# Kernel optimization log

Hardware: AMD Instinct MI355X
Metric: run time of the kernel (lower is better)

## Reference

```python
import jax, jax.numpy as jnp
import numpy as np
import math

B, L, D, H = 2, 2048, 1024, 16

def setup_inputs() -> dict:
    key = jax.random.key(0)
    ks = jax.random.split(key, 5)
    return {
        "query": jax.random.normal(ks[0], (B, L, D), dtype=jnp.float32),
        "key": jax.random.normal(ks[1], (B, L, D), dtype=jnp.float32),
        "value": jax.random.normal(ks[2], (B, L, D), dtype=jnp.float32),
        "w_out": jax.random.normal(ks[3], (D, D), dtype=jnp.float32) * (1.0 / math.sqrt(D)),
        "b_out": jnp.zeros((D,), dtype=jnp.float32),
    }

def reference(query, key, value, w_out, b_out):
    b, l, d_model = query.shape
    num_heads = H
    head_dim = d_model // num_heads
    scaling = 1.0 / math.sqrt(d_model)  # NOTE: module scales by embed_dim, not head_dim

    def reshape(x):
        return x.reshape(b, l, num_heads, head_dim).transpose(0, 2, 1, 3)  # [B,H,L,hd]

    q, k, v = reshape(query), reshape(key), reshape(value)
    scores = jnp.einsum("bhqd,bhkd->bhqk", q, k) * scaling  # [B,H,L,L]

    u = max(1, int(math.ceil(math.log(l + 1))))  # static: 8 for L=2048
    _, topk_idx = jax.lax.top_k(scores, u)  # [B,H,L,u]

    # scatter True at top-u key positions per query
    bi = jnp.arange(b)[:, None, None, None]
    hi = jnp.arange(num_heads)[None, :, None, None]
    qi = jnp.arange(l)[None, None, :, None]
    mask = jnp.zeros(scores.shape, dtype=bool).at[bi, hi, qi, topk_idx].set(True)

    scores_masked = jnp.where(mask, scores, -jnp.inf)
    attn_weights = jax.nn.softmax(scores_masked, axis=-1)  # [B,H,L,L]

    attn_out = jnp.einsum("bhqk,bhkd->bhqd", attn_weights, v)
    attn_out = attn_out.transpose(0, 2, 1, 3).reshape(b, l, d_model)
    attn_out = attn_out @ w_out.T + b_out  # nn.Linear
    return attn_out, attn_weights
```

## Files before the change

kernel.cpp:

```cpp
#include <hip/hip_runtime.h>
#include <math.h>

#define BB 2
#define LL 2048
#define DD 1024
#define HH 16
#define SCALE 0.03125f

#define ATTN_ELEMS ((size_t)BB * LL * DD)

typedef unsigned short u16;
typedef __attribute__((ext_vector_type(8))) short bf16x8;
typedef __attribute__((ext_vector_type(4))) short s16x4;
typedef __attribute__((ext_vector_type(4))) float f32x4;

__device__ __forceinline__ u16 f2bf_rne(float f) {
    union { float f; unsigned u; } c; c.f = f;
    unsigned u = c.u;
    u += 0x7fffu + ((u >> 16) & 1u);
    return (u16)(u >> 16);
}

__device__ __forceinline__ void splitbf(float x, short& h, short& l) {
    union { float f; unsigned u; } c; c.f = x;
    unsigned uh = c.u & 0xFFFF0000u;
    h = (short)(uh >> 16);
    union { unsigned u; float f; } ch; ch.u = uh;
    l = (short)f2bf_rne(x - ch.f);
}

__device__ __forceinline__ void insert8(float (&tv)[8], int (&ti)[8], float cv, int ci) {
    bool g0 = cv > tv[0], g1 = cv > tv[1], g2 = cv > tv[2], g3 = cv > tv[3],
         g4 = cv > tv[4], g5 = cv > tv[5], g6 = cv > tv[6];
    tv[7] = g6 ? tv[6] : cv;                 ti[7] = g6 ? ti[6] : ci;
    tv[6] = g5 ? tv[5] : (g6 ? cv : tv[6]);  ti[6] = g5 ? ti[5] : (g6 ? ci : ti[6]);
    tv[5] = g4 ? tv[4] : (g5 ? cv : tv[5]);  ti[5] = g4 ? ti[4] : (g5 ? ci : ti[5]);
    tv[4] = g3 ? tv[3] : (g4 ? cv : tv[4]);  ti[4] = g3 ? ti[3] : (g4 ? ci : ti[4]);
    tv[3] = g2 ? tv[2] : (g3 ? cv : tv[3]);  ti[3] = g2 ? ti[2] : (g3 ? ci : ti[3]);
    tv[2] = g1 ? tv[1] : (g2 ? cv : tv[2]);  ti[2] = g1 ? ti[1] : (g2 ? ci : ti[2]);
    tv[1] = g0 ? tv[0] : (g1 ? cv : tv[1]);  ti[1] = g0 ? ti[0] : (g1 ? ci : ti[1]);
    tv[0] = g0 ? cv : tv[0];                 ti[0] = g0 ? ci : ti[0];
}

__device__ __forceinline__ void insert8t(float (&tv)[8], int (&ti)[8], float cv, int ci) {
    bool g0 = cv > tv[0] || (cv == tv[0] && ci < ti[0]);
    bool g1 = cv > tv[1] || (cv == tv[1] && ci < ti[1]);
    bool g2 = cv > tv[2] || (cv == tv[2] && ci < ti[2]);
    bool g3 = cv > tv[3] || (cv == tv[3] && ci < ti[3]);
    bool g4 = cv > tv[4] || (cv == tv[4] && ci < ti[4]);
    bool g5 = cv > tv[5] || (cv == tv[5] && ci < ti[5]);
    bool g6 = cv > tv[6] || (cv == tv[6] && ci < ti[6]);
    tv[7] = g6 ? tv[6] : cv;                 ti[7] = g6 ? ti[6] : ci;
    tv[6] = g5 ? tv[5] : (g6 ? cv : tv[6]);  ti[6] = g5 ? ti[5] : (g6 ? ci : ti[6]);
    tv[5] = g4 ? tv[4] : (g5 ? cv : tv[5]);  ti[5] = g4 ? ti[4] : (g5 ? ci : ti[5]);
    tv[4] = g3 ? tv[3] : (g4 ? cv : tv[4]);  ti[4] = g3 ? ti[3] : (g4 ? ci : ti[4]);
    tv[3] = g2 ? tv[2] : (g3 ? cv : tv[3]);  ti[3] = g2 ? ti[2] : (g3 ? ci : ti[3]);
    tv[2] = g1 ? tv[1] : (g2 ? cv : tv[2]);  ti[2] = g1 ? ti[1] : (g2 ? ci : ti[2]);
    tv[1] = g0 ? tv[0] : (g1 ? cv : tv[1]);  ti[1] = g0 ? ti[0] : (g1 ? ci : ti[1]);
    tv[0] = g0 ? cv : tv[0];                 ti[0] = g0 ? ci : ti[0];
}

__device__ __forceinline__ void insert12(float (&tv)[12], int (&ti)[12], float cv, int ci) {
    bool g0 = cv > tv[0], g1 = cv > tv[1], g2 = cv > tv[2], g3 = cv > tv[3],
         g4 = cv > tv[4], g5 = cv > tv[5], g6 = cv > tv[6], g7 = cv > tv[7],
         g8 = cv > tv[8], g9 = cv > tv[9], g10 = cv > tv[10];
    tv[11] = g10 ? tv[10] : cv;                 ti[11] = g10 ? ti[10] : ci;
    tv[10] = g9 ? tv[9] : (g10 ? cv : tv[10]);  ti[10] = g9 ? ti[9] : (g10 ? ci : ti[10]);
    tv[9]  = g8 ? tv[8] : (g9 ? cv : tv[9]);    ti[9]  = g8 ? ti[8] : (g9 ? ci : ti[9]);
    tv[8]  = g7 ? tv[7] : (g8 ? cv : tv[8]);    ti[8]  = g7 ? ti[7] : (g8 ? ci : ti[8]);
    tv[7]  = g6 ? tv[6] : (g7 ? cv : tv[7]);    ti[7]  = g6 ? ti[6] : (g7 ? ci : ti[7]);
    tv[6]  = g5 ? tv[5] : (g6 ? cv : tv[6]);    ti[6]  = g5 ? ti[5] : (g6 ? ci : ti[6]);
    tv[5]  = g4 ? tv[4] : (g5 ? cv : tv[5]);    ti[5]  = g4 ? ti[4] : (g5 ? ci : ti[5]);
    tv[4]  = g3 ? tv[3] : (g4 ? cv : tv[4]);    ti[4]  = g3 ? ti[3] : (g4 ? ci : ti[4]);
    tv[3]  = g2 ? tv[2] : (g3 ? cv : tv[3]);    ti[3]  = g2 ? ti[2] : (g3 ? ci : ti[3]);
    tv[2]  = g1 ? tv[1] : (g2 ? cv : tv[2]);    ti[2]  = g1 ? ti[1] : (g2 ? ci : ti[2]);
    tv[1]  = g0 ? tv[0] : (g1 ? cv : tv[1]);    ti[1]  = g0 ? ti[0] : (g1 ? ci : ti[1]);
    tv[0]  = g0 ? cv : tv[0];                   ti[0]  = g0 ? ci : ti[0];
}

__device__ __forceinline__ void merge4(
    const float* v0, const int* i0, const float* v1, const int* i1,
    const float* v2, const int* i2, const float* v3, const int* i3,
    float* ov, int* oi)
{
    int p0 = 0, p1 = 0, p2 = 0, p3 = 0;
    #pragma unroll
    for (int s = 0; s < 8; ++s) {
        float a0 = v0[p0], a1 = v1[p1], a2 = v2[p2], a3 = v3[p3];
        int   b0 = i0[p0], b1 = i1[p1], b2 = i2[p2], b3 = i3[p3];
        float bv = a0; int bi = b0; int bc = 0;
        if (a1 > bv || (a1 == bv && b1 < bi)) { bv = a1; bi = b1; bc = 1; }
        if (a2 > bv || (a2 == bv && b2 < bi)) { bv = a2; bi = b2; bc = 2; }
        if (a3 > bv || (a3 == bv && b3 < bi)) { bv = a3; bi = b3; bc = 3; }
        p0 += (bc == 0); p1 += (bc == 1); p2 += (bc == 2); p3 += (bc == 3);
        ov[s] = bv; oi[s] = bi;
    }
}


__global__ __launch_bounds__(256) void prep_k_kernel(
    const float* __restrict__ k, u16* __restrict__ khi, u16* __restrict__ klo)
{
    int gid = blockIdx.x * 256 + threadIdx.x;
    int li   = gid & 15;
    int qd   = (gid >> 4) & 3;
    int c    = (gid >> 6) & 1;
    int s    = (gid >> 7) & 127;
    int head = gid >> 14;
    int b = head >> 4, h = head & 15;
    const float* src = k + ((size_t)(b * LL + s * 16 + li)) * DD + h * 64 + c * 32 + qd * 8;
    float x[8];
    *(f32x4*)x       = *(const f32x4*)src;
    *(f32x4*)(x + 4) = *(const f32x4*)(src + 4);
    bf16x8 h8, l8;
    #pragma unroll
    for (int e = 0; e < 8; ++e) { short hh, ll; splitbf(x[e], hh, ll); h8[e] = hh; l8[e] = ll; }
    *(bf16x8*)&khi[(size_t)gid * 8] = h8;
    *(bf16x8*)&klo[(size_t)gid * 8] = l8;
}

__global__ __launch_bounds__(256) void prep_w_kernel(
    const float* __restrict__ w, u16* __restrict__ whi, u16* __restrict__ wlo)
{
    int gid = blockIdx.x * 256 + threadIdx.x;
    int li = gid & 15;
    int qd = (gid >> 4) & 3;
    int c  = (gid >> 6) & 3;
    int nt = (gid >> 8) & 3;
    int kc = (gid >> 10) & 7;
    int nb = gid >> 13;
    const float* src = w + (size_t)(nb * 64 + nt * 16 + li) * DD + kc * 128 + c * 32 + qd * 8;
    float x[8];
    *(f32x4*)x       = *(const f32x4*)src;
    *(f32x4*)(x + 4) = *(const f32x4*)(src + 4);
    bf16x8 h8, l8;
    #pragma unroll
    for (int e = 0; e < 8; ++e) { short hh, ll; splitbf(x[e], hh, ll); h8[e] = hh; l8[e] = ll; }
    *(bf16x8*)&whi[(size_t)gid * 8] = h8;
    *(bf16x8*)&wlo[(size_t)gid * 8] = l8;
}

__global__ __launch_bounds__(256, 4) void attn_fast_kernel(
    const float* __restrict__ q, const float* __restrict__ k, const float* __restrict__ v,
    const u16* __restrict__ khi_g, const u16* __restrict__ klo_g,
    float* __restrict__ aw, u16* __restrict__ chi, u16* __restrict__ clo)
{
    const int swz  = (blockIdx.x & 7) * 128 + (blockIdx.x >> 3);
    const int qt   = swz & 31;
    const int h    = (swz >> 5) & 15;
    const int b    = swz >> 9;
    const int t    = threadIdx.x;
    const int wv   = t >> 6;
    const int lane = t & 63;
    const int li   = lane & 15;
    const int quad = lane >> 4;

    __shared__ __align__(16) char arena[21504];
    u16*   gsel = (u16*)(arena);
    float* dv   = (float*)(arena + 1536);
    u16*   dg   = (u16*)(arena + 13824);
    float* s2v  = (float*)(arena + 1536);
    u16*   s2i  = (u16*)(arena + 13824);
    float* wrow = (float*)(arena + 18432);
    u16*   wixs = (u16*)(arena + 20480);

    f32x4* awz = (f32x4*)(aw + (((size_t)(b * HH + h) * LL) + (size_t)qt * 64) * LL);
    const f32x4 zero4 = {0.f, 0.f, 0.f, 0.f};

    bf16x8 qh0, ql0, qh1, ql1;
    {
        const float* qrow = q + ((size_t)(b * LL + qt * 64 + wv * 16 + li)) * DD + h * 64;
        float x[8];
        *(f32x4*)x       = *(const f32x4*)(qrow + quad * 8);
        *(f32x4*)(x + 4) = *(const f32x4*)(qrow + quad * 8 + 4);
        #pragma unroll
        for (int e = 0; e < 8; ++e) { short hh, ll; splitbf(x[e], hh, ll); qh0[e] = hh; ql0[e] = ll; }
        *(f32x4*)x       = *(const f32x4*)(qrow + 32 + quad * 8);
        *(f32x4*)(x + 4) = *(const f32x4*)(qrow + 32 + quad * 8 + 4);
        #pragma unroll
        for (int e = 0; e < 8; ++e) { short hh, ll; splitbf(x[e], hh, ll); qh1[e] = hh; ql1[e] = ll; }
    }

    float tv[12]; int tg[12];
    #pragma unroll
    for (int s = 0; s < 12; ++s) { tv[s] = -INFINITY; tg[s] = 0; }

    const u16* khb = khi_g + (size_t)(b * HH + h) * 131072 + (size_t)lane * 8;
    const u16* klb = klo_g + (size_t)(b * HH + h) * 131072 + (size_t)lane * 8;

    bf16x8 Ah0 = *(const bf16x8*)(khb);
    bf16x8 Ah1 = *(const bf16x8*)(khb + 512);
    bf16x8 Al0 = *(const bf16x8*)(klb);
    bf16x8 Al1 = *(const bf16x8*)(klb + 512);
    bf16x8 Bh0 = *(const bf16x8*)(khb + 1024);
    bf16x8 Bh1 = *(const bf16x8*)(khb + 1536);
    bf16x8 Bl0 = *(const bf16x8*)(klb + 1024);
    bf16x8 Bl1 = *(const bf16x8*)(klb + 1536);

    #pragma unroll 2
    for (int sp = 0; sp < 64; ++sp) {
        const int spn = (sp + 1) & 63;
        const size_t off = (size_t)spn * 2048;
        bf16x8 NAh0 = *(const bf16x8*)(khb + off);
        bf16x8 NAh1 = *(const bf16x8*)(khb + off + 512);
        bf16x8 NAl0 = *(const bf16x8*)(klb + off);
        bf16x8 NAl1 = *(const bf16x8*)(klb + off + 512);
        bf16x8 NBh0 = *(const bf16x8*)(khb + off + 1024);
        bf16x8 NBh1 = *(const bf16x8*)(khb + off + 1536);
        bf16x8 NBl0 = *(const bf16x8*)(klb + off + 1024);
        bf16x8 NBl1 = *(const bf16x8*)(klb + off + 1536);

        awz[sp * 512 + t]       = zero4;
        awz[sp * 512 + 256 + t] = zero4;

        f32x4 c4a = {0,0,0,0}, c4b = {0,0,0,0}, d4a = {0,0,0,0}, d4b = {0,0,0,0};
        c4a = __builtin_amdgcn_mfma_f32_16x16x32_bf16(Ah0, qh0, c4a, 0, 0, 0);
        c4b = __builtin_amdgcn_mfma_f32_16x16x32_bf16(Ah1, qh1, c4b, 0, 0, 0);
        d4a = __builtin_amdgcn_mfma_f32_16x16x32_bf16(Bh0, qh0, d4a, 0, 0, 0);
        d4b = __builtin_amdgcn_mfma_f32_16x16x32_bf16(Bh1, qh1, d4b, 0, 0, 0);
        c4a = __builtin_amdgcn_mfma_f32_16x16x32_bf16(Al0, qh0, c4a, 0, 0, 0);
        c4b = __builtin_amdgcn_mfma_f32_16x16x32_bf16(Al1, qh1, c4b, 0, 0, 0);
        d4a = __builtin_amdgcn_mfma_f32_16x16x32_bf16(Bl0, qh0, d4a, 0, 0, 0);
        d4b = __builtin_amdgcn_mfma_f32_16x16x32_bf16(Bl1, qh1, d4b, 0, 0, 0);
        c4a = __builtin_amdgcn_mfma_f32_16x16x32_bf16(Ah0, ql0, c4a, 0, 0, 0);
        c4b = __builtin_amdgcn_mfma_f32_16x16x32_bf16(Ah1, ql1, c4b, 0, 0, 0);
        d4a = __builtin_amdgcn_mfma_f32_16x16x32_bf16(Bh0, ql0, d4a, 0, 0, 0);
        d4b = __builtin_amdgcn_mfma_f32_16x16x32_bf16(Bh1, ql1, d4b, 0, 0, 0);

        float s0 = c4a[0] + c4b[0], s1 = c4a[1] + c4b[1];
        float s2 = c4a[2] + c4b[2], s3 = c4a[3] + c4b[3];
        float s4 = d4a[0] + d4b[0], s5 = d4a[1] + d4b[1];
        float s6 = d4a[2] + d4b[2], s7 = d4a[3] + d4b[3];
        float m = fmaxf(fmaxf(fmaxf(s0, s1), fmaxf(s2, s3)),
                        fmaxf(fmaxf(s4, s5), fmaxf(s6, s7)));
        if (m > tv[11]) insert12(tv, tg, m, sp * 32 + quad * 4);

        Ah0 = NAh0; Ah1 = NAh1; Al0 = NAl0; Al1 = NAl1;
        Bh0 = NBh0; Bh1 = NBh1; Bl0 = NBl0; Bl1 = NBl1;
    }

    {
        const int row = wv * 16 + li;
        #pragma unroll
        for (int s = 0; s < 12; ++s) {
            dv[row * 48 + quad * 12 + s] = tv[s];
            dg[row * 48 + quad * 12 + s] = (u16)tg[s];
        }
    }
    __syncthreads();

    if (t < 64) {
        const float* v0 = &dv[t * 48];       const u16* i0 = &dg[t * 48];
        const float* v1 = &dv[t * 48 + 12];  const u16* i1 = &dg[t * 48 + 12];
        const float* v2 = &dv[t * 48 + 24];  const u16* i2 = &dg[t * 48 + 24];
        const float* v3 = &dv[t * 48 + 36];  const u16* i3 = &dg[t * 48 + 36];
        int p0 = 0, p1 = 0, p2 = 0, p3 = 0;
        #pragma unroll
        for (int s = 0; s < 12; ++s) {
            float a0 = v0[p0], a1 = v1[p1], a2 = v2[p2], a3 = v3[p3];
            int   b0 = i0[p0], b1 = i1[p1], b2 = i2[p2], b3 = i3[p3];
            float bv = a0; int bi = b0; int bc = 0;
            if (a1 > bv || (a1 == bv && b1 < bi)) { bv = a1; bi = b1; bc = 1; }
            if (a2 > bv || (a2 == bv && b2 < bi)) { bv = a2; bi = b2; bc = 2; }
            if (a3 > bv || (a3 == bv && b3 < bi)) { bv = a3; bi = b3; bc = 3; }
            p0 += (bc == 0); p1 += (bc == 1); p2 += (bc == 2); p3 += (bc == 3);
            gsel[t * 12 + s] = (u16)bi;
        }
    }
    __syncthreads();

    {
        const int row = t >> 2, p = t & 3;
        const float* qp = q + ((size_t)(b * LL + qt * 64 + row)) * DD + h * 64;
        f32x4 qr[16];
        #pragma unroll
        for (int d4 = 0; d4 < 16; ++d4) qr[d4] = *(const f32x4*)(qp + d4 * 4);
        float tv8[8]; int ti8[8];
        #pragma unroll
        for (int s = 0; s < 8; ++s) { tv8[s] = -INFINITY; ti8[s] = 0x7fffffff; }
        for (int jj = 0; jj < 24; jj += 2) {
            int gk = (int)gsel[row * 12 + p * 3 + (jj >> 3)];
            int e  = jj & 7;
            int k0 = gk + ((e >> 2) << 4) + (e & 3);
            int k1 = k0 + 1;
            const float* kp0 = k + ((size_t)(b * LL + k0)) * DD + h * 64;
            const float* kp1 = k + ((size_t)(b * LL + k1)) * DD + h * 64;
            float a0 = 0.f, a1 = 0.f, a2 = 0.f, a3 = 0.f;
            float b0 = 0.f, b1 = 0.f, b2 = 0.f, b3 = 0.f;
            #pragma unroll
            for (int d4 = 0; d4 < 16; ++d4) {
                f32x4 ka = *(const f32x4*)(kp0 + d4 * 4);
                f32x4 kb = *(const f32x4*)(kp1 + d4 * 4);
                a0 = fmaf(qr[d4][0], ka[0], a0);
                a1 = fmaf(qr[d4][1], ka[1], a1);
                a2 = fmaf(qr[d4][2], ka[2], a2);
                a3 = fmaf(qr[d4][3], ka[3], a3);
                b0 = fmaf(qr[d4][0], kb[0], b0);
                b1 = fmaf(qr[d4][1], kb[1], b1);
                b2 = fmaf(qr[d4][2], kb[2], b2);
                b3 = fmaf(qr[d4][3], kb[3], b3);
            }
            float sc0 = ((a0 + a1) + (a2 + a3)) * SCALE;
            float sc1 = ((b0 + b1) + (b2 + b3)) * SCALE;
            if (sc0 > tv8[7] || (sc0 == tv8[7] && k0 < ti8[7])) insert8t(tv8, ti8, sc0, k0);
            if (sc1 > tv8[7] || (sc1 == tv8[7] && k1 < ti8[7])) insert8t(tv8, ti8, sc1, k1);
        }
        #pragma unroll
        for (int s = 0; s < 8; ++s) {
            s2v[(row * 4 + p) * 9 + s] = tv8[s];
            s2i[(row * 4 + p) * 9 + s] = (u16)ti8[s];
        }
    }
    __syncthreads();

    if (t < 64) {
        const float* v0 = &s2v[(t * 4 + 0) * 9]; const u16* i0 = &s2i[(t * 4 + 0) * 9];
        const float* v1 = &s2v[(t * 4 + 1) * 9]; const u16* i1 = &s2i[(t * 4 + 1) * 9];
        const float* v2 = &s2v[(t * 4 + 2) * 9]; const u16* i2 = &s2i[(t * 4 + 2) * 9];
        const float* v3 = &s2v[(t * 4 + 3) * 9]; const u16* i3 = &s2i[(t * 4 + 3) * 9];
        int p0 = 0, p1 = 0, p2 = 0, p3 = 0;
        float fv[8]; int fi[8];
        #pragma unroll
        for (int s = 0; s < 8; ++s) {
            float a0 = v0[p0], a1 = v1[p1], a2 = v2[p2], a3 = v3[p3];
            int   b0 = i0[p0], b1 = i1[p1], b2 = i2[p2], b3 = i3[p3];
            float bv = a0; int bi = b0; int bc = 0;
            if (a1 > bv || (a1 == bv && b1 < bi)) { bv = a1; bi = b1; bc = 1; }
            if (a2 > bv || (a2 == bv && b2 < bi)) { bv = a2; bi = b2; bc = 2; }
            if (a3 > bv || (a3 == bv && b3 < bi)) { bv = a3; bi = b3; bc = 3; }
            p0 += (bc == 0); p1 += (bc == 1); p2 += (bc == 2); p3 += (bc == 3);
            fv[s] = bv; fi[s] = bi;
        }
        float m = fv[0];
        float e0[8]; float sum = 0.f;
        #pragma unroll
        for (int s = 0; s < 8; ++s) { e0[s] = __expf(fv[s] - m); sum += e0[s]; }
        float inv = 1.0f / sum;
        float* awrow = aw + (((size_t)(b * HH + h) * LL) + (size_t)qt * 64 + t) * LL;
        #pragma unroll
        for (int s = 0; s < 8; ++s) {
            float w8 = e0[s] * inv;
            awrow[fi[s]] = w8;
            wrow[t * 8 + s] = w8; wixs[t * 8 + s] = (u16)fi[s];
        }
    }
    __syncthreads();

    const float* vbase = v + ((size_t)b * LL) * DD + h * 64;
    #pragma unroll
    for (int i = 0; i < 4; ++i) {
        int id = i * 256 + t;
        int row = id >> 4, seg = id & 15;
        f32x4 acc = {0.f, 0.f, 0.f, 0.f};
        #pragma unroll
        for (int s = 0; s < 8; ++s) {
            float ws = wrow[row * 8 + s];
            f32x4 vvv = *(const f32x4*)(vbase + (size_t)wixs[row * 8 + s] * DD + seg * 4);
            acc[0] = fmaf(ws, vvv[0], acc[0]);
            acc[1] = fmaf(ws, vvv[1], acc[1]);
            acc[2] = fmaf(ws, vvv[2], acc[2]);
            acc[3] = fmaf(ws, vvv[3], acc[3]);
        }
        size_t off = ((size_t)(b * LL + qt * 64 + row)) * DD + h * 64 + seg * 4;
        s16x4 h4, l4;
        #pragma unroll
        for (int j = 0; j < 4; ++j) { short hh, ll; splitbf(acc[j], hh, ll); h4[j] = hh; l4[j] = ll; }
        *(s16x4*)(chi + off) = h4;
        *(s16x4*)(clo + off) = l4;
    }
}

__global__ __launch_bounds__(256) void linear_fast_kernel(
    const u16* __restrict__ chi, const u16* __restrict__ clo,
    const u16* __restrict__ whi, const u16* __restrict__ wlo,
    const float* __restrict__ bias, float* __restrict__ out)
{
    const int bid  = blockIdx.x;
    const int nb   = bid & 15, mb = bid >> 4;
    const int t    = threadIdx.x;
    const int wv   = t >> 6;
    const int lane = t & 63;
    const int li   = lane & 15;
    const int quad = lane >> 4;

    f32x4 acc0 = {0.f,0.f,0.f,0.f}, acc1 = {0.f,0.f,0.f,0.f},
          acc2 = {0.f,0.f,0.f,0.f}, acc3 = {0.f,0.f,0.f,0.f};

    const u16* ah_row = chi + (size_t)(mb * 64 + wv * 16 + li) * DD + quad * 8;
    const u16* al_row = clo + (size_t)(mb * 64 + wv * 16 + li) * DD + quad * 8;
    const size_t wboff = (size_t)nb * 65536 + (size_t)lane * 8;

    for (int kc = 0; kc < 8; ++kc) {
        const u16* wb_h = whi + wboff + kc * 8192;
        const u16* wb_l = wlo + wboff + kc * 8192;
        #pragma unroll
        for (int c = 0; c < 4; ++c) {
            bf16x8 ah = *(const bf16x8*)(ah_row + kc * 128 + c * 32);
            bf16x8 al = *(const bf16x8*)(al_row + kc * 128 + c * 32);
            bf16x8 bh0 = *(const bf16x8*)(wb_h + c * 512);
            bf16x8 bl0 = *(const bf16x8*)(wb_l + c * 512);
            bf16x8 bh1 = *(const bf16x8*)(wb_h + 2048 + c * 512);
            bf16x8 bl1 = *(const bf16x8*)(wb_l + 2048 + c * 512);
            bf16x8 bh2 = *(const bf16x8*)(wb_h + 4096 + c * 512);
            bf16x8 bl2 = *(const bf16x8*)(wb_l + 4096 + c * 512);
            bf16x8 bh3 = *(const bf16x8*)(wb_h + 6144 + c * 512);
            bf16x8 bl3 = *(const bf16x8*)(wb_l + 6144 + c * 512);
            acc0 = __builtin_amdgcn_mfma_f32_16x16x32_bf16(ah, bh0, acc0, 0, 0, 0);
            acc0 = __builtin_amdgcn_mfma_f32_16x16x32_bf16(ah, bl0, acc0, 0, 0, 0);
            acc0 = __builtin_amdgcn_mfma_f32_16x16x32_bf16(al, bh0, acc0, 0, 0, 0);
            acc1 = __builtin_amdgcn_mfma_f32_16x16x32_bf16(ah, bh1, acc1, 0, 0, 0);
            acc1 = __builtin_amdgcn_mfma_f32_16x16x32_bf16(ah, bl1, acc1, 0, 0, 0);
            acc1 = __builtin_amdgcn_mfma_f32_16x16x32_bf16(al, bh1, acc1, 0, 0, 0);
            acc2 = __builtin_amdgcn_mfma_f32_16x16x32_bf16(ah, bh2, acc2, 0, 0, 0);
            acc2 = __builtin_amdgcn_mfma_f32_16x16x32_bf16(ah, bl2, acc2, 0, 0, 0);
            acc2 = __builtin_amdgcn_mfma_f32_16x16x32_bf16(al, bh2, acc2, 0, 0, 0);
            acc3 = __builtin_amdgcn_mfma_f32_16x16x32_bf16(ah, bh3, acc3, 0, 0, 0);
            acc3 = __builtin_amdgcn_mfma_f32_16x16x32_bf16(ah, bl3, acc3, 0, 0, 0);
            acc3 = __builtin_amdgcn_mfma_f32_16x16x32_bf16(al, bh3, acc3, 0, 0, 0);
        }
    }

    #pragma unroll
    for (int st = 0; st < 4; ++st) {
        f32x4 a = (st == 0) ? acc0 : (st == 1) ? acc1 : (st == 2) ? acc2 : acc3;
        int col = nb * 64 + st * 16 + li;
        float bb2 = bias[col];
        #pragma unroll
        for (int r = 0; r < 4; ++r)
            out[(size_t)(mb * 64 + wv * 16 + quad * 4 + r) * DD + col] = a[r] + bb2;
    }
}


__global__ __launch_bounds__(256) void attn_kernel(
    const float* __restrict__ q, const float* __restrict__ k, const float* __restrict__ v,
    float* __restrict__ aw, float* __restrict__ ctx)
{
    const int bid  = blockIdx.x;
    const int qt   = bid & 31;
    const int h    = (bid >> 5) & 15;
    const int b    = bid >> 9;
    const int t    = threadIdx.x;
    const int wv   = t >> 6;
    const int lane = t & 63;
    const int li   = lane & 15;
    const int quad = lane >> 4;

    __shared__ __align__(16) char smA[32768];
    __shared__ float s2v[32][4][8];
    __shared__ int   s2i[32][4][8];
    __shared__ int   cidx[32][12];
    __shared__ float cs[32][12];
    __shared__ float wrow[64][8];
    __shared__ int   wix[64][8];
    u16* khi = (u16*)smA;
    u16* klo = (u16*)(smA + 16384);

    const float* kbase = k + ((size_t)b * LL) * DD + h * 64;
    f32x4* awz = (f32x4*)(aw + (((size_t)(b * HH + h) * LL) + (size_t)qt * 64) * LL);
    const f32x4 zero4 = {0.f, 0.f, 0.f, 0.f};

    bf16x8 qh0, ql0, qh1, ql1;
    {
        const float* qrow = q + ((size_t)(b * LL + qt * 64 + wv * 16 + li)) * DD + h * 64;
        float x[8];
        *(f32x4*)x       = *(const f32x4*)(qrow + quad * 8);
        *(f32x4*)(x + 4) = *(const f32x4*)(qrow + quad * 8 + 4);
        #pragma unroll
        for (int e = 0; e < 8; ++e) { short hh, ll; splitbf(x[e], hh, ll); qh0[e] = hh; ql0[e] = ll; }
        *(f32x4*)x       = *(const f32x4*)(qrow + 32 + quad * 8);
        *(f32x4*)(x + 4) = *(const f32x4*)(qrow + 32 + quad * 8 + 4);
        #pragma unroll
        for (int e = 0; e < 8; ++e) { short hh, ll; splitbf(x[e], hh, ll); qh1[e] = hh; ql1[e] = ll; }
    }

    float tv[4][8]; int tix[4][8];
    #pragma unroll
    for (int r = 0; r < 4; ++r)
        #pragma unroll
        for (int s = 0; s < 8; ++s) { tv[r][s] = -INFINITY; tix[r][s] = 0; }

    for (int iter = 0; iter < 16; ++iter) {
        __syncthreads();
        #pragma unroll
        for (int j = 0; j < 4; ++j) {
            int f   = j * 256 + t;
            int col = f >> 3;
            int c   = (f >> 2) & 1;
            int qd  = f & 3;
            const float* src = kbase + (size_t)(iter * 128 + col) * DD + c * 32 + qd * 8;
            float x[8];
            *(f32x4*)x       = *(const f32x4*)src;
            *(f32x4*)(x + 4) = *(const f32x4*)(src + 4);
            bf16x8 h8, l8;
            #pragma unroll
            for (int e = 0; e < 8; ++e) { short hh, ll; splitbf(x[e], hh, ll); h8[e] = hh; l8[e] = ll; }
            int off = (((col >> 4) * 2 + c) << 9) + (qd << 7) + ((col & 15) << 3);
            *(bf16x8*)&khi[off] = h8;
            *(bf16x8*)&klo[off] = l8;
        }
        #pragma unroll
        for (int i = 0; i < 8; ++i) awz[iter * 2048 + i * 256 + t] = zero4;
        __syncthreads();

        #pragma unroll
        for (int s = 0; s < 8; ++s) {
            int fo = s << 10;
            bf16x8 kh0 = *(bf16x8*)&khi[fo + (lane << 3)];
            bf16x8 kh1 = *(bf16x8*)&khi[fo + 512 + (lane << 3)];
            bf16x8 kl0 = *(bf16x8*)&klo[fo + (lane << 3)];
            bf16x8 kl1 = *(bf16x8*)&klo[fo + 512 + (lane << 3)];
            f32x4 c4 = {0.f, 0.f, 0.f, 0.f};
            c4 = __builtin_amdgcn_mfma_f32_16x16x32_bf16(qh0, kh0, c4, 0, 0, 0);
            c4 = __builtin_amdgcn_mfma_f32_16x16x32_bf16(qh1, kh1, c4, 0, 0, 0);
            c4 = __builtin_amdgcn_mfma_f32_16x16x32_bf16(qh0, kl0, c4, 0, 0, 0);
            c4 = __builtin_amdgcn_mfma_f32_16x16x32_bf16(qh1, kl1, c4, 0, 0, 0);
            c4 = __builtin_amdgcn_mfma_f32_16x16x32_bf16(ql0, kh0, c4, 0, 0, 0);
            c4 = __builtin_amdgcn_mfma_f32_16x16x32_bf16(ql1, kh1, c4, 0, 0, 0);
            int ci = iter * 128 + s * 16 + li;
            #pragma unroll
            for (int r = 0; r < 4; ++r) {
                float cv = c4[r] * SCALE;
                if (cv > tv[r][7]) insert8(tv[r], tix[r], cv, ci);
            }
        }
    }

    float* mv = (float*)smA;
    int*   mi = (int*)(smA + 16384);
    for (int bb = 0; bb < 2; ++bb) {
        __syncthreads();
        if ((wv >> 1) == bb) {
            int rl0 = (wv & 1) * 16 + quad * 4;
            #pragma unroll
            for (int r = 0; r < 4; ++r) {
                int base = (rl0 + r) * 128 + li * 8;
                #pragma unroll
                for (int s = 0; s < 8; ++s) { mv[base + s] = tv[r][s]; mi[base + s] = tix[r][s]; }
            }
        }
        __syncthreads();
        if (t < 128) {
            int rr = t >> 2, p = t & 3;
            int base = rr * 128 + p * 32;
            merge4(&mv[base], &mi[base], &mv[base + 8], &mi[base + 8],
                   &mv[base + 16], &mi[base + 16], &mv[base + 24], &mi[base + 24],
                   s2v[rr][p], s2i[rr][p]);
        }
        __syncthreads();
        if (t < 32) {
            int rr = t;
            int pp[4] = {0, 0, 0, 0};
            #pragma unroll
            for (int s = 0; s < 12; ++s) {
                float bv = -INFINITY; int bi = 0x7fffffff; int bc = 0;
                #pragma unroll
                for (int l = 0; l < 4; ++l) {
                    if (pp[l] < 8) {
                        float hv = s2v[rr][l][pp[l]]; int hi2 = s2i[rr][l][pp[l]];
                        if (hv > bv || (hv == bv && hi2 < bi)) { bv = hv; bi = hi2; bc = l; }
                    }
                }
                pp[bc] += 1;
                cidx[rr][s] = bi;
            }
        }
        __syncthreads();
        for (int task = t; task < 384; task += 256) {
            int row = task / 12, c = task - row * 12;
            const float* qp = q + ((size_t)(b * LL + qt * 64 + bb * 32 + row)) * DD + h * 64;
            const float* kp = k + ((size_t)(b * LL + cidx[row][c])) * DD + h * 64;
            float acc = 0.f;
            for (int d4 = 0; d4 < 16; ++d4) {
                f32x4 qa = *(const f32x4*)(qp + d4 * 4);
                f32x4 ka = *(const f32x4*)(kp + d4 * 4);
                acc = fmaf(qa[0], ka[0], acc);
                acc = fmaf(qa[1], ka[1], acc);
                acc = fmaf(qa[2], ka[2], acc);
                acc = fmaf(qa[3], ka[3], acc);
            }
            cs[row][c] = acc * SCALE;
        }
        __syncthreads();
        if (t < 32) {
            int rr = t;
            float vv[12]; int ii[12];
            #pragma unroll
            for (int c = 0; c < 12; ++c) { vv[c] = cs[rr][c]; ii[c] = cidx[rr][c]; }
            float fv[8]; int fi[8];
            #pragma unroll
            for (int s = 0; s < 8; ++s) {
                float bv = -INFINITY; int bi = 0x7fffffff; int bc = 0;
                #pragma unroll
                for (int c = 0; c < 12; ++c) {
                    if (vv[c] > bv || (vv[c] == bv && ii[c] < bi)) { bv = vv[c]; bi = ii[c]; bc = c; }
                }
                vv[bc] = -INFINITY;
                fv[s] = bv; fi[s] = bi;
            }
            float m = fv[0];
            float e0[8]; float sum = 0.f;
            #pragma unroll
            for (int s = 0; s < 8; ++s) { e0[s] = __expf(fv[s] - m); sum += e0[s]; }
            float inv = 1.0f / sum;
            int grow = bb * 32 + rr;
            float* awrow = aw + (((size_t)(b * HH + h) * LL) + (size_t)qt * 64 + grow) * LL;
            #pragma unroll
            for (int s = 0; s < 8; ++s) {
                float w8 = e0[s] * inv;
                awrow[fi[s]] = w8;
                wrow[grow][s] = w8; wix[grow][s] = fi[s];
            }
        }
    }
    __syncthreads();

    const float* vbase = v + ((size_t)b * LL) * DD + h * 64;
    #pragma unroll
    for (int i = 0; i < 4; ++i) {
        int id = i * 256 + t;
        int row = id >> 4, seg = id & 15;
        f32x4 acc = {0.f, 0.f, 0.f, 0.f};
        #pragma unroll
        for (int s = 0; s < 8; ++s) {
            float ws = wrow[row][s];
            f32x4 vvv = *(const f32x4*)(vbase + (size_t)wix[row][s] * DD + seg * 4);
            acc[0] = fmaf(ws, vvv[0], acc[0]);
            acc[1] = fmaf(ws, vvv[1], acc[1]);
            acc[2] = fmaf(ws, vvv[2], acc[2]);
            acc[3] = fmaf(ws, vvv[3], acc[3]);
        }
        *(f32x4*)(ctx + ((size_t)(b * LL + qt * 64 + row)) * DD + h * 64 + seg * 4) = acc;
    }
}

__global__ __launch_bounds__(256) void linear_ws_kernel(
    const float* __restrict__ ctx, const float* __restrict__ w,
    const float* __restrict__ bias, float* __restrict__ out)
{
    const int bid  = blockIdx.x;
    const int nb   = bid & 15, mb = bid >> 4;
    const int t    = threadIdx.x;
    const int wv   = t >> 6;
    const int lane = t & 63;
    const int li   = lane & 15;
    const int quad = lane >> 4;

    __shared__ u16 bhi[8192], blo[8192];

    f32x4 acc0 = {0.f,0.f,0.f,0.f}, acc1 = {0.f,0.f,0.f,0.f},
          acc2 = {0.f,0.f,0.f,0.f}, acc3 = {0.f,0.f,0.f,0.f};
    const float* arow = ctx + (size_t)(mb * 64 + wv * 16 + li) * DD;

    for (int kc = 0; kc < 8; ++kc) {
        __syncthreads();
        #pragma unroll
        for (int j = 0; j < 4; ++j) {
            int f   = j * 256 + t;
            int col = f >> 4;
            int c   = (f >> 2) & 3;
            int qd  = f & 3;
            const float* src = w + (size_t)(nb * 64 + col) * DD + kc * 128 + c * 32 + qd * 8;
            float x[8];
            *(f32x4*)x       = *(const f32x4*)src;
            *(f32x4*)(x + 4) = *(const f32x4*)(src + 4);
            bf16x8 h8, l8;
            #pragma unroll
            for (int e = 0; e < 8; ++e) { short hh, ll; splitbf(x[e], hh, ll); h8[e] = hh; l8[e] = ll; }
            int off = (((col >> 4) * 4 + c) << 9) + (qd << 7) + ((col & 15) << 3);
            *(bf16x8*)&bhi[off] = h8;
            *(bf16x8*)&blo[off] = l8;
        }
        __syncthreads();

        bf16x8 ah[4], al[4];
        #pragma unroll
        for (int c = 0; c < 4; ++c) {
            float x[8];
            *(f32x4*)x       = *(const f32x4*)(arow + kc * 128 + c * 32 + quad * 8);
            *(f32x4*)(x + 4) = *(const f32x4*)(arow + kc * 128 + c * 32 + quad * 8 + 4);
            #pragma unroll
            for (int e = 0; e < 8; ++e) { short hh, ll; splitbf(x[e], hh, ll); ah[c][e] = hh; al[c][e] = ll; }
        }
        #pragma unroll
        for (int c = 0; c < 4; ++c) {
            bf16x8 bh0 = *(bf16x8*)&bhi[(( 0 + c) << 9) + (lane << 3)];
            bf16x8 bl0 = *(bf16x8*)&blo[(( 0 + c) << 9) + (lane << 3)];
            bf16x8 bh1 = *(bf16x8*)&bhi[(( 4 + c) << 9) + (lane << 3)];
            bf16x8 bl1 = *(bf16x8*)&blo[(( 4 + c) << 9) + (lane << 3)];
            bf16x8 bh2 = *(bf16x8*)&bhi[(( 8 + c) << 9) + (lane << 3)];
            bf16x8 bl2 = *(bf16x8*)&blo[(( 8 + c) << 9) + (lane << 3)];
            bf16x8 bh3 = *(bf16x8*)&bhi[((12 + c) << 9) + (lane << 3)];
            bf16x8 bl3 = *(bf16x8*)&blo[((12 + c) << 9) + (lane << 3)];
            acc0 = __builtin_amdgcn_mfma_f32_16x16x32_bf16(ah[c], bh0, acc0, 0, 0, 0);
            acc0 = __builtin_amdgcn_mfma_f32_16x16x32_bf16(ah[c], bl0, acc0, 0, 0, 0);
            acc0 = __builtin_amdgcn_mfma_f32_16x16x32_bf16(al[c], bh0, acc0, 0, 0, 0);
            acc1 = __builtin_amdgcn_mfma_f32_16x16x32_bf16(ah[c], bh1, acc1, 0, 0, 0);
            acc1 = __builtin_amdgcn_mfma_f32_16x16x32_bf16(ah[c], bl1, acc1, 0, 0, 0);
            acc1 = __builtin_amdgcn_mfma_f32_16x16x32_bf16(al[c], bh1, acc1, 0, 0, 0);
            acc2 = __builtin_amdgcn_mfma_f32_16x16x32_bf16(ah[c], bh2, acc2, 0, 0, 0);
            acc2 = __builtin_amdgcn_mfma_f32_16x16x32_bf16(ah[c], bl2, acc2, 0, 0, 0);
            acc2 = __builtin_amdgcn_mfma_f32_16x16x32_bf16(al[c], bh2, acc2, 0, 0, 0);
            acc3 = __builtin_amdgcn_mfma_f32_16x16x32_bf16(ah[c], bh3, acc3, 0, 0, 0);
            acc3 = __builtin_amdgcn_mfma_f32_16x16x32_bf16(ah[c], bl3, acc3, 0, 0, 0);
            acc3 = __builtin_amdgcn_mfma_f32_16x16x32_bf16(al[c], bh3, acc3, 0, 0, 0);
        }
    }

    #pragma unroll
    for (int st = 0; st < 4; ++st) {
        f32x4 a = (st == 0) ? acc0 : (st == 1) ? acc1 : (st == 2) ? acc2 : acc3;
        int col = nb * 64 + st * 16 + li;
        float bb2 = bias[col];
        #pragma unroll
        for (int r = 0; r < 4; ++r)
            out[(size_t)(mb * 64 + wv * 16 + quad * 4 + r) * DD + col] = a[r] + bb2;
    }
}

__global__ __launch_bounds__(256) void linear_inplace_kernel(
    float* io, const float* __restrict__ w, const float* __restrict__ bias)
{
    __shared__ u16 ahi[16384], alo[16384];
    const int t    = threadIdx.x;
    const int m0   = blockIdx.x * 16;
    const int wv   = t >> 6;
    const int lane = t & 63;
    const int li   = lane & 15;
    const int quad = lane >> 4;

    #pragma unroll
    for (int i = 0; i < 8; ++i) {
        int id  = i * 256 + t;
        int row = id >> 7;
        int c   = (id >> 2) & 31;
        int qd  = id & 3;
        const float* src = io + (size_t)(m0 + row) * DD + c * 32 + qd * 8;
        float x[8];
        *(f32x4*)x       = *(const f32x4*)src;
        *(f32x4*)(x + 4) = *(const f32x4*)(src + 4);
        bf16x8 h8, l8;
        #pragma unroll
        for (int e = 0; e < 8; ++e) { short hh, ll; splitbf(x[e], hh, ll); h8[e] = hh; l8[e] = ll; }
        int off = (c << 9) + (qd << 7) + (row << 3);
        *(bf16x8*)&ahi[off] = h8;
        *(bf16x8*)&alo[off] = l8;
    }
    __syncthreads();

    f32x4 acc[16];
    #pragma unroll
    for (int i = 0; i < 16; ++i) acc[i] = (f32x4){0.f, 0.f, 0.f, 0.f};

    for (int c = 0; c < 32; ++c) {
        bf16x8 ah = *(bf16x8*)&ahi[(c << 9) + (lane << 3)];
        bf16x8 al = *(bf16x8*)&alo[(c << 9) + (lane << 3)];
        #pragma unroll
        for (int sub = 0; sub < 16; ++sub) {
            int col = wv * 256 + sub * 16 + li;
            const float* src = w + (size_t)col * DD + c * 32 + quad * 8;
            float x[8];
            *(f32x4*)x       = *(const f32x4*)src;
            *(f32x4*)(x + 4) = *(const f32x4*)(src + 4);
            bf16x8 bh, bl;
            #pragma unroll
            for (int e = 0; e < 8; ++e) { short hh, ll; splitbf(x[e], hh, ll); bh[e] = hh; bl[e] = ll; }
            acc[sub] = __builtin_amdgcn_mfma_f32_16x16x32_bf16(ah, bh, acc[sub], 0, 0, 0);
            acc[sub] = __builtin_amdgcn_mfma_f32_16x16x32_bf16(ah, bl, acc[sub], 0, 0, 0);
            acc[sub] = __builtin_amdgcn_mfma_f32_16x16x32_bf16(al, bh, acc[sub], 0, 0, 0);
        }
    }

    #pragma unroll
    for (int sub = 0; sub < 16; ++sub) {
        int col = wv * 256 + sub * 16 + li;
        float bb2 = bias[col];
        #pragma unroll
        for (int r = 0; r < 4; ++r)
            io[(size_t)(m0 + quad * 4 + r) * DD + col] = acc[sub][r] + bb2;
    }
}

extern "C" void kernel_launch(void* const* d_in, const int* in_sizes, int n_in,
                              void* d_out, int out_size, void* d_ws, size_t ws_size,
                              hipStream_t stream) {
    const float* q    = (const float*)d_in[0];
    const float* k    = (const float*)d_in[1];
    const float* v    = (const float*)d_in[2];
    const float* w    = (const float*)d_in[3];
    const float* bias = (const float*)d_in[4];

    float* out = (float*)d_out;
    float* aw  = out + ATTN_ELEMS;

    const size_t CHI_ELE = ATTN_ELEMS;
    const size_t KSP_ELE = 4194304;
    const size_t WSP_ELE = 1048576;
    const size_t need_fast = (2 * CHI_ELE + 2 * KSP_ELE + 2 * WSP_ELE) * sizeof(u16);

    if (d_ws != nullptr && ws_size >= need_fast) {
        u16* chi = (u16*)d_ws;
        u16* clo = chi + CHI_ELE;
        u16* khi = clo + CHI_ELE;
        u16* klo = khi + KSP_ELE;
        u16* whi = klo + KSP_ELE;
        u16* wlo = whi + WSP_ELE;
        prep_k_kernel<<<2048, 256, 0, stream>>>(k, khi, klo);
        prep_w_kernel<<<512, 256, 0, stream>>>(w, whi, wlo);
        attn_fast_kernel<<<BB * HH * (LL / 64), 256, 0, stream>>>(q, k, v, khi, klo, aw, chi, clo);
        linear_fast_kernel<<<(BB * LL / 64) * (DD / 64), 256, 0, stream>>>(chi, clo, whi, wlo, bias, out);
    } else {
        const bool use_ws = (d_ws != nullptr) && (ws_size >= ATTN_ELEMS * sizeof(float));
        float* ctx = use_ws ? (float*)d_ws : out;
        attn_kernel<<<BB * HH * (LL / 64), 256, 0, stream>>>(q, k, v, aw, ctx);
        if (use_ws) {
            linear_ws_kernel<<<(BB * LL / 64) * (DD / 64), 256, 0, stream>>>(ctx, w, bias, out);
        } else {
            linear_inplace_kernel<<<BB * LL / 16, 256, 0, stream>>>(out, w, bias);
        }
    }
}
```

Measured before the change: 1.093 ms.

## Stage key tiles through double-buffered LDS shared by all waves

Each of the four waves previously streamed the full packed key hi/lo data from global memory on its own. Now each wave loads a quarter of every 64-key tile into a double-buffered shared-memory area, and all waves read the tile from LDS, with the next tile prefetched into registers. This cuts global/L2 traffic for keys by roughly four times, at the cost of a block barrier per tile and 32KB of shared memory. The launch-bounds occupancy hint of 4 blocks per CU is also dropped.

```diff
diff --git a/kernel.cpp b/kernel.cpp
--- a/kernel.cpp
+++ b/kernel.cpp
@@ -140,7 +140,7 @@
     *(bf16x8*)&wlo[(size_t)gid * 8] = l8;
 }
 
-__global__ __launch_bounds__(256, 4) void attn_fast_kernel(
+__global__ __launch_bounds__(256) void attn_fast_kernel(
     const float* __restrict__ q, const float* __restrict__ k, const float* __restrict__ v,
     const u16* __restrict__ khi_g, const u16* __restrict__ klo_g,
     float* __restrict__ aw, u16* __restrict__ chi, u16* __restrict__ clo)
@@ -155,14 +155,16 @@
     const int li   = lane & 15;
     const int quad = lane >> 4;
 
-    __shared__ __align__(16) char arena[21504];
-    u16*   gsel = (u16*)(arena);
-    float* dv   = (float*)(arena + 1536);
-    u16*   dg   = (u16*)(arena + 13824);
-    float* s2v  = (float*)(arena + 1536);
-    u16*   s2i  = (u16*)(arena + 13824);
-    float* wrow = (float*)(arena + 18432);
-    u16*   wixs = (u16*)(arena + 20480);
+    __shared__ __align__(16) char smem[32768];
+    u16*   kb0  = (u16*)(smem);
+    u16*   kb1  = (u16*)(smem + 16384);
+    u16*   gsel = (u16*)(smem);
+    float* dv   = (float*)(smem + 1536);
+    u16*   dg   = (u16*)(smem + 13824);
+    float* s2v  = (float*)(smem + 1536);
+    u16*   s2i  = (u16*)(smem + 13824);
+    float* wrow = (float*)(smem + 18432);
+    u16*   wixs = (u16*)(smem + 20480);
 
     f32x4* awz = (f32x4*)(aw + (((size_t)(b * HH + h) * LL) + (size_t)qt * 64) * LL);
     const f32x4 zero4 = {0.f, 0.f, 0.f, 0.f};
@@ -188,55 +190,81 @@
     const u16* khb = khi_g + (size_t)(b * HH + h) * 131072 + (size_t)lane * 8;
     const u16* klb = klo_g + (size_t)(b * HH + h) * 131072 + (size_t)lane * 8;
 
-    bf16x8 Ah0 = *(const bf16x8*)(khb);
-    bf16x8 Ah1 = *(const bf16x8*)(khb + 512);
-    bf16x8 Al0 = *(const bf16x8*)(klb);
-    bf16x8 Al1 = *(const bf16x8*)(klb + 512);
-    bf16x8 Bh0 = *(const bf16x8*)(khb + 1024);
-    bf16x8 Bh1 = *(const bf16x8*)(khb + 1536);
-    bf16x8 Bl0 = *(const bf16x8*)(klb + 1024);
-    bf16x8 Bl1 = *(const bf16x8*)(klb + 1536);
-
-    #pragma unroll 2
-    for (int sp = 0; sp < 64; ++sp) {
-        const int spn = (sp + 1) & 63;
-        const size_t off = (size_t)spn * 2048;
-        bf16x8 NAh0 = *(const bf16x8*)(khb + off);
-        bf16x8 NAh1 = *(const bf16x8*)(khb + off + 512);
-        bf16x8 NAl0 = *(const bf16x8*)(klb + off);
-        bf16x8 NAl1 = *(const bf16x8*)(klb + off + 512);
-        bf16x8 NBh0 = *(const bf16x8*)(khb + off + 1024);
-        bf16x8 NBh1 = *(const bf16x8*)(khb + off + 1536);
-        bf16x8 NBl0 = *(const bf16x8*)(klb + off + 1024);
-        bf16x8 NBl1 = *(const bf16x8*)(klb + off + 1536);
-
-        awz[sp * 512 + t]       = zero4;
-        awz[sp * 512 + 256 + t] = zero4;
-
-        f32x4 c4a = {0,0,0,0}, c4b = {0,0,0,0}, d4a = {0,0,0,0}, d4b = {0,0,0,0};
-        c4a = __builtin_amdgcn_mfma_f32_16x16x32_bf16(Ah0, qh0, c4a, 0, 0, 0);
-        c4b = __builtin_amdgcn_mfma_f32_16x16x32_bf16(Ah1, qh1, c4b, 0, 0, 0);
-        d4a = __builtin_amdgcn_mfma_f32_16x16x32_bf16(Bh0, qh0, d4a, 0, 0, 0);
-        d4b = __builtin_amdgcn_mfma_f32_16x16x32_bf16(Bh1, qh1, d4b, 0, 0, 0);
-        c4a = __builtin_amdgcn_mfma_f32_16x16x32_bf16(Al0, qh0, c4a, 0, 0, 0);
-        c4b = __builtin_amdgcn_mfma_f32_16x16x32_bf16(Al1, qh1, c4b, 0, 0, 0);
-        d4a = __builtin_amdgcn_mfma_f32_16x16x32_bf16(Bl0, qh0, d4a, 0, 0, 0);
-        d4b = __builtin_amdgcn_mfma_f32_16x16x32_bf16(Bl1, qh1, d4b, 0, 0, 0);
-        c4a = __builtin_amdgcn_mfma_f32_16x16x32_bf16(Ah0, ql0, c4a, 0, 0, 0);
-        c4b = __builtin_amdgcn_mfma_f32_16x16x32_bf16(Ah1, ql1, c4b, 0, 0, 0);
-        d4a = __builtin_amdgcn_mfma_f32_16x16x32_bf16(Bh0, ql0, d4a, 0, 0, 0);
-        d4b = __builtin_amdgcn_mfma_f32_16x16x32_bf16(Bh1, ql1, d4b, 0, 0, 0);
-
-        float s0 = c4a[0] + c4b[0], s1 = c4a[1] + c4b[1];
-        float s2 = c4a[2] + c4b[2], s3 = c4a[3] + c4b[3];
-        float s4 = d4a[0] + d4b[0], s5 = d4a[1] + d4b[1];
-        float s6 = d4a[2] + d4b[2], s7 = d4a[3] + d4b[3];
-        float m = fmaxf(fmaxf(fmaxf(s0, s1), fmaxf(s2, s3)),
-                        fmaxf(fmaxf(s4, s5), fmaxf(s6, s7)));
-        if (m > tv[11]) insert12(tv, tg, m, sp * 32 + quad * 4);
-
-        Ah0 = NAh0; Ah1 = NAh1; Al0 = NAl0; Al1 = NAl1;
-        Bh0 = NBh0; Bh1 = NBh1; Bl0 = NBl0; Bl1 = NBl1;
+    {
+        const size_t g = (size_t)wv * 1024;
+        bf16x8 r0 = *(const bf16x8*)(khb + g);
+        bf16x8 r1 = *(const bf16x8*)(khb + g + 512);
+        bf16x8 r2 = *(const bf16x8*)(klb + g);
+        bf16x8 r3 = *(const bf16x8*)(klb + g + 512);
+        u16* dst = kb0 + wv * 2048 + lane * 8;
+        *(bf16x8*)(dst)        = r0;
+        *(bf16x8*)(dst + 512)  = r1;
+        *(bf16x8*)(dst + 1024) = r2;
+        *(bf16x8*)(dst + 1536) = r3;
+    }
+    __syncthreads();
+
+    int cur = 0;
+    for (int tile = 0; tile < 32; ++tile) {
+        bf16x8 r0, r1, r2, r3;
+        const bool pf = (tile < 31);
+        if (pf) {
+            const size_t g = ((size_t)(tile + 1) * 4 + wv) * 1024;
+            r0 = *(const bf16x8*)(khb + g);
+            r1 = *(const bf16x8*)(khb + g + 512);
+            r2 = *(const bf16x8*)(klb + g);
+            r3 = *(const bf16x8*)(klb + g + 512);
+        }
+        #pragma unroll
+        for (int z = 0; z < 4; ++z) awz[tile * 1024 + z * 256 + t] = zero4;
+
+        const u16* base = cur ? kb1 : kb0;
+        #pragma unroll
+        for (int p = 0; p < 2; ++p) {
+            const int soA = (2 * p) * 2048 + lane * 8;
+            const int soB = (2 * p + 1) * 2048 + lane * 8;
+            bf16x8 Ah0 = *(const bf16x8*)(base + soA);
+            bf16x8 Ah1 = *(const bf16x8*)(base + soA + 512);
+            bf16x8 Al0 = *(const bf16x8*)(base + soA + 1024);
+            bf16x8 Al1 = *(const bf16x8*)(base + soA + 1536);
+            bf16x8 Bh0 = *(const bf16x8*)(base + soB);
+            bf16x8 Bh1 = *(const bf16x8*)(base + soB + 512);
+            bf16x8 Bl0 = *(const bf16x8*)(base + soB + 1024);
+            bf16x8 Bl1 = *(const bf16x8*)(base + soB + 1536);
+
+            f32x4 c4a = {0,0,0,0}, c4b = {0,0,0,0}, d4a = {0,0,0,0}, d4b = {0,0,0,0};
+            c4a = __builtin_amdgcn_mfma_f32_16x16x32_bf16(Ah0, qh0, c4a, 0, 0, 0);
+            c4b = __builtin_amdgcn_mfma_f32_16x16x32_bf16(Ah1, qh1, c4b, 0, 0, 0);
+            d4a = __builtin_amdgcn_mfma_f32_16x16x32_bf16(Bh0, qh0, d4a, 0, 0, 0);
+            d4b = __builtin_amdgcn_mfma_f32_16x16x32_bf16(Bh1, qh1, d4b, 0, 0, 0);
+            c4a = __builtin_amdgcn_mfma_f32_16x16x32_bf16(Al0, qh0, c4a, 0, 0, 0);
+            c4b = __builtin_amdgcn_mfma_f32_16x16x32_bf16(Al1, qh1, c4b, 0, 0, 0);
+            d4a = __builtin_amdgcn_mfma_f32_16x16x32_bf16(Bl0, qh0, d4a, 0, 0, 0);
+            d4b = __builtin_amdgcn_mfma_f32_16x16x32_bf16(Bl1, qh1, d4b, 0, 0, 0);
+            c4a = __builtin_amdgcn_mfma_f32_16x16x32_bf16(Ah0, ql0, c4a, 0, 0, 0);
+            c4b = __builtin_amdgcn_mfma_f32_16x16x32_bf16(Ah1, ql1, c4b, 0, 0, 0);
+            d4a = __builtin_amdgcn_mfma_f32_16x16x32_bf16(Bh0, ql0, d4a, 0, 0, 0);
+            d4b = __builtin_amdgcn_mfma_f32_16x16x32_bf16(Bh1, ql1, d4b, 0, 0, 0);
+
+            float s0 = c4a[0] + c4b[0], s1 = c4a[1] + c4b[1];
+            float s2 = c4a[2] + c4b[2], s3 = c4a[3] + c4b[3];
+            float s4 = d4a[0] + d4b[0], s5 = d4a[1] + d4b[1];
+            float s6 = d4a[2] + d4b[2], s7 = d4a[3] + d4b[3];
+            float m = fmaxf(fmaxf(fmaxf(s0, s1), fmaxf(s2, s3)),
+                            fmaxf(fmaxf(s4, s5), fmaxf(s6, s7)));
+            const int sp = tile * 2 + p;
+            if (m > tv[11]) insert12(tv, tg, m, sp * 32 + quad * 4);
+        }
+
+        if (pf) {
+            u16* dst = (cur ? kb0 : kb1) + wv * 2048 + lane * 8;
+            *(bf16x8*)(dst)        = r0;
+            *(bf16x8*)(dst + 512)  = r1;
+            *(bf16x8*)(dst + 1024) = r2;
+            *(bf16x8*)(dst + 1536) = r3;
+        }
+        __syncthreads();
+        cur ^= 1;
     }
 
     {
```

Measured after the change: 910.3 us. 1.2x faster.

## Split attention top-k scan into four key-chunk blocks with a separate finalize kernel

Applied to the files above, without the earlier changes.

Splits the single fused attention kernel into a scan kernel launched with four times as many blocks, each handling a quarter of the key range and writing per-chunk top-12 candidates into scratch space inside the attention-weights output. A new finalize kernel reads those candidates, merges them, clears the scratch region, then does the softmax, the V gather and the context write. Zeroing of the large attention-weights tensor moves from per-block stores inside the scan loop to a single hipMemsetAsync. The aim is more parallelism and a lighter scan loop, at the cost of an extra launch, a global round trip for candidates, and dropping the software prefetch of K.

```diff
diff --git a/kernel.cpp b/kernel.cpp
--- a/kernel.cpp
+++ b/kernel.cpp
@@ -8,8 +8,10 @@
 #define SCALE 0.03125f
 
 #define ATTN_ELEMS ((size_t)BB * LL * DD)
+#define AW_ELEMS ((size_t)BB * HH * LL * LL)
 
 typedef unsigned short u16;
+typedef unsigned int u32;
 typedef __attribute__((ext_vector_type(8))) short bf16x8;
 typedef __attribute__((ext_vector_type(4))) short s16x4;
 typedef __attribute__((ext_vector_type(4))) float f32x4;
@@ -140,32 +142,26 @@
     *(bf16x8*)&wlo[(size_t)gid * 8] = l8;
 }
 
-__global__ __launch_bounds__(256, 4) void attn_fast_kernel(
-    const float* __restrict__ q, const float* __restrict__ k, const float* __restrict__ v,
+__global__ __launch_bounds__(256) void attn_scan_kernel(
+    const float* __restrict__ q,
     const u16* __restrict__ khi_g, const u16* __restrict__ klo_g,
-    float* __restrict__ aw, u16* __restrict__ chi, u16* __restrict__ clo)
+    float* __restrict__ aw)
 {
-    const int swz  = (blockIdx.x & 7) * 128 + (blockIdx.x >> 3);
-    const int qt   = swz & 31;
-    const int h    = (swz >> 5) & 15;
-    const int b    = swz >> 9;
-    const int t    = threadIdx.x;
-    const int wv   = t >> 6;
-    const int lane = t & 63;
-    const int li   = lane & 15;
-    const int quad = lane >> 4;
-
-    __shared__ __align__(16) char arena[21504];
-    u16*   gsel = (u16*)(arena);
-    float* dv   = (float*)(arena + 1536);
-    u16*   dg   = (u16*)(arena + 13824);
-    float* s2v  = (float*)(arena + 1536);
-    u16*   s2i  = (u16*)(arena + 13824);
-    float* wrow = (float*)(arena + 18432);
-    u16*   wixs = (u16*)(arena + 20480);
-
-    f32x4* awz = (f32x4*)(aw + (((size_t)(b * HH + h) * LL) + (size_t)qt * 64) * LL);
-    const f32x4 zero4 = {0.f, 0.f, 0.f, 0.f};
+    const int raw   = blockIdx.x;
+    const int chunk = raw >> 10;
+    const int crest = raw & 1023;
+    const int swz   = (crest & 7) * 128 + (crest >> 3);
+    const int qt    = swz & 31;
+    const int h     = (swz >> 5) & 15;
+    const int b     = swz >> 9;
+    const int t     = threadIdx.x;
+    const int wv    = t >> 6;
+    const int lane  = t & 63;
+    const int li    = lane & 15;
+    const int quad  = lane >> 4;
+
+    __shared__ float dv[64 * 48];
+    __shared__ u16   dg[64 * 48];
 
     bf16x8 qh0, ql0, qh1, ql1;
     {
@@ -188,30 +184,18 @@
     const u16* khb = khi_g + (size_t)(b * HH + h) * 131072 + (size_t)lane * 8;
     const u16* klb = klo_g + (size_t)(b * HH + h) * 131072 + (size_t)lane * 8;
 
-    bf16x8 Ah0 = *(const bf16x8*)(khb);
-    bf16x8 Ah1 = *(const bf16x8*)(khb + 512);
-    bf16x8 Al0 = *(const bf16x8*)(klb);
-    bf16x8 Al1 = *(const bf16x8*)(klb + 512);
-    bf16x8 Bh0 = *(const bf16x8*)(khb + 1024);
-    bf16x8 Bh1 = *(const bf16x8*)(khb + 1536);
-    bf16x8 Bl0 = *(const bf16x8*)(klb + 1024);
-    bf16x8 Bl1 = *(const bf16x8*)(klb + 1536);
-
     #pragma unroll 2
-    for (int sp = 0; sp < 64; ++sp) {
-        const int spn = (sp + 1) & 63;
-        const size_t off = (size_t)spn * 2048;
-        bf16x8 NAh0 = *(const bf16x8*)(khb + off);
-        bf16x8 NAh1 = *(const bf16x8*)(khb + off + 512);
-        bf16x8 NAl0 = *(const bf16x8*)(klb + off);
-        bf16x8 NAl1 = *(const bf16x8*)(klb + off + 512);
-        bf16x8 NBh0 = *(const bf16x8*)(khb + off + 1024);
-        bf16x8 NBh1 = *(const bf16x8*)(khb + off + 1536);
-        bf16x8 NBl0 = *(const bf16x8*)(klb + off + 1024);
-        bf16x8 NBl1 = *(const bf16x8*)(klb + off + 1536);
-
-        awz[sp * 512 + t]       = zero4;
-        awz[sp * 512 + 256 + t] = zero4;
+    for (int i = 0; i < 16; ++i) {
+        const int sp = chunk * 16 + i;
+        const size_t off = (size_t)sp * 2048;
+        bf16x8 Ah0 = *(const bf16x8*)(khb + off);
+        bf16x8 Ah1 = *(const bf16x8*)(khb + off + 512);
+        bf16x8 Al0 = *(const bf16x8*)(klb + off);
+        bf16x8 Al1 = *(const bf16x8*)(klb + off + 512);
+        bf16x8 Bh0 = *(const bf16x8*)(khb + off + 1024);
+        bf16x8 Bh1 = *(const bf16x8*)(khb + off + 1536);
+        bf16x8 Bl0 = *(const bf16x8*)(klb + off + 1024);
+        bf16x8 Bl1 = *(const bf16x8*)(klb + off + 1536);
 
         f32x4 c4a = {0,0,0,0}, c4b = {0,0,0,0}, d4a = {0,0,0,0}, d4b = {0,0,0,0};
         c4a = __builtin_amdgcn_mfma_f32_16x16x32_bf16(Ah0, qh0, c4a, 0, 0, 0);
@@ -234,9 +218,6 @@
         float m = fmaxf(fmaxf(fmaxf(s0, s1), fmaxf(s2, s3)),
                         fmaxf(fmaxf(s4, s5), fmaxf(s6, s7)));
         if (m > tv[11]) insert12(tv, tg, m, sp * 32 + quad * 4);
-
-        Ah0 = NAh0; Ah1 = NAh1; Al0 = NAl0; Al1 = NAl1;
-        Bh0 = NBh0; Bh1 = NBh1; Bl0 = NBl0; Bl1 = NBl1;
     }
 
     {
@@ -248,6 +229,63 @@
         }
     }
     __syncthreads();
+
+    if (t < 64) {
+        float* sv = aw + (size_t)swz * 131072;
+        u32*   si = (u32*)(sv + 3072);
+        const float* v0 = &dv[t * 48];       const u16* i0 = &dg[t * 48];
+        const float* v1 = &dv[t * 48 + 12];  const u16* i1 = &dg[t * 48 + 12];
+        const float* v2 = &dv[t * 48 + 24];  const u16* i2 = &dg[t * 48 + 24];
+        const float* v3 = &dv[t * 48 + 36];  const u16* i3 = &dg[t * 48 + 36];
+        int p0 = 0, p1 = 0, p2 = 0, p3 = 0;
+        #pragma unroll
+        for (int s = 0; s < 12; ++s) {
+            float a0 = v0[p0], a1 = v1[p1], a2 = v2[p2], a3 = v3[p3];
+            int   b0 = i0[p0], b1 = i1[p1], b2 = i2[p2], b3 = i3[p3];
+            float bv = a0; int bi = b0; int bc = 0;
+            if (a1 > bv || (a1 == bv && b1 < bi)) { bv = a1; bi = b1; bc = 1; }
+            if (a2 > bv || (a2 == bv && b2 < bi)) { bv = a2; bi = b2; bc = 2; }
+            if (a3 > bv || (a3 == bv && b3 < bi)) { bv = a3; bi = b3; bc = 3; }
+            p0 += (bc == 0); p1 += (bc == 1); p2 += (bc == 2); p3 += (bc == 3);
+            sv[t * 48 + chunk * 12 + s] = bv;
+            si[t * 48 + chunk * 12 + s] = (u32)bi;
+        }
+    }
+}
+
+__global__ __launch_bounds__(256) void attn_finalize_kernel(
+    const float* __restrict__ q, const float* __restrict__ k, const float* __restrict__ v,
+    float* __restrict__ aw, u16* __restrict__ chi, u16* __restrict__ clo)
+{
+    const int swz  = (blockIdx.x & 7) * 128 + (blockIdx.x >> 3);
+    const int qt   = swz & 31;
+    const int h    = (swz >> 5) & 15;
+    const int b    = swz >> 9;
+    const int t    = threadIdx.x;
+
+    __shared__ __align__(16) char arena[21504];
+    u16*   gsel = (u16*)(arena);
+    float* dv   = (float*)(arena + 1536);
+    u16*   dg   = (u16*)(arena + 13824);
+    float* s2v  = (float*)(arena + 1536);
+    u16*   s2i  = (u16*)(arena + 13824);
+    float* wrow = (float*)(arena + 18432);
+    u16*   wixs = (u16*)(arena + 20480);
+
+    float* sv = aw + (size_t)swz * 131072;
+    u32*   si = (u32*)(sv + 3072);
+    const f32x4 zero4 = {0.f, 0.f, 0.f, 0.f};
+
+    for (int i = t; i < 3072; i += 256) {
+        dv[i] = sv[i];
+        dg[i] = (u16)si[i];
+    }
+    __syncthreads();
+
+    {
+        f32x4* zz = (f32x4*)sv;
+        for (int i = t; i < 1536; i += 256) zz[i] = zero4;
+    }
 
     if (t < 64) {
         const float* v0 = &dv[t * 48];       const u16* i0 = &dg[t * 48];
@@ -346,6 +384,8 @@
     }
     __syncthreads();
 
+    const int lane = t & 63;
+    (void)lane;
     const float* vbase = v + ((size_t)b * LL) * DD + h * 64;
     #pragma unroll
     for (int i = 0; i < 4; ++i) {
@@ -805,9 +845,11 @@
         u16* klo = khi + KSP_ELE;
         u16* whi = klo + KSP_ELE;
         u16* wlo = whi + WSP_ELE;
+        hipMemsetAsync(aw, 0, AW_ELEMS * sizeof(float), stream);
         prep_k_kernel<<<2048, 256, 0, stream>>>(k, khi, klo);
         prep_w_kernel<<<512, 256, 0, stream>>>(w, whi, wlo);
-        attn_fast_kernel<<<BB * HH * (LL / 64), 256, 0, stream>>>(q, k, v, khi, klo, aw, chi, clo);
+        attn_scan_kernel<<<4096, 256, 0, stream>>>(q, khi, klo, aw);
+        attn_finalize_kernel<<<1024, 256, 0, stream>>>(q, k, v, aw, chi, clo);
         linear_fast_kernel<<<(BB * LL / 64) * (DD / 64), 256, 0, stream>>>(chi, clo, whi, wlo, bias, out);
     } else {
         const bool use_ws = (d_ws != nullptr) && (ws_size >= ATTN_ELEMS * sizeof(float));
```

After: 957.0 us. 12.4% less time.
